# Performance work log

Hardware: AMD Instinct MI355X
Metric: run time of the kernel (lower is better)

Reference implementation:

```python
import jax, jax.numpy as jnp
import numpy as np

HID = 256  # hidden_dim


def setup_inputs() -> dict:
    key = jax.random.key(0)
    ks = jax.random.split(key, 8)
    B, C, H, W = 256, 1, 1024, 64
    D = W  # input_dim
    scale = 0.05
    return {
        "x": jax.random.normal(ks[0], (B, C, H, W), jnp.float32),
        "h0": jax.random.normal(ks[1], (B, HID), jnp.float32),
        "c0": jax.random.normal(ks[2], (B, HID), jnp.float32),
        "Wi": jax.random.normal(ks[3], (4 * HID, D), jnp.float32) * scale,
        "bi": jnp.zeros((4 * HID,), jnp.float32),
        "Wh": jax.random.normal(ks[4], (4 * HID, HID), jnp.float32) * scale,
        "bh": jnp.zeros((4 * HID,), jnp.float32),
        "Wcls": jax.random.normal(ks[5], (10, HID), jnp.float32) * scale,
        "bcls": jnp.zeros((10,), jnp.float32),
    }


def reference(x, h0, c0, Wi, bi, Wh, bh, Wcls, bcls):
    B, C, H, W = x.shape
    S = C * H  # seq_length
    seq = x.reshape(B, S, W)
    # precompute input-to-gate projections for all timesteps: [B,S,4H]
    xg = jnp.einsum("bsd,gd->bsg", seq, Wi) + bi

    def step(carry, xg_t):
        h, c = carry
        g = xg_t + h @ Wh.T + bh  # [B,4H], gate order: f,i,g,o
        f = jax.nn.sigmoid(g[:, 0 * HID:1 * HID])
        i = jax.nn.sigmoid(g[:, 1 * HID:2 * HID])
        gg = jnp.tanh(g[:, 2 * HID:3 * HID])
        o = jax.nn.sigmoid(g[:, 3 * HID:4 * HID])
        c_new = c * f + i * gg
        h_new = jnp.tanh(c_new) * o
        return (h_new, c_new), None

    (h_last, _), _ = jax.lax.scan(step, (h0, c0), jnp.swapaxes(xg, 0, 1))
    # classifier on last hidden state
    return h_last @ Wcls.T + bcls
```

## Files before the change

### kernel.cpp

```cpp
#include <hip/hip_runtime.h>

#define SEQ   1024
#define DIN   64
#define NHID  256
#define NBLK  64
#define NTHR  512

typedef _Float16 f16x8 __attribute__((ext_vector_type(8)));
typedef float    f32x4 __attribute__((ext_vector_type(4)));
typedef unsigned long long u64;

#define MFMA16(a,b,c) __builtin_amdgcn_mfma_f32_16x16x32_f16((a),(b),(c),0,0,0)

__device__ __forceinline__ float sigm(float v){
  return __builtin_amdgcn_rcpf(1.f + __expf(-v));
}
__device__ __forceinline__ float tanh_f(float v){
  return 1.f - 2.f*__builtin_amdgcn_rcpf(__expf(2.f*v)+1.f);
}

__device__ __forceinline__ f16x8 cvt8(f32x4 a, f32x4 b){
  f16x8 r;
  r[0]=(_Float16)a[0]; r[1]=(_Float16)a[1]; r[2]=(_Float16)a[2]; r[3]=(_Float16)a[3];
  r[4]=(_Float16)b[0]; r[5]=(_Float16)b[1]; r[6]=(_Float16)b[2]; r[7]=(_Float16)b[3];
  return r;
}

union U32H2 { unsigned int u; _Float16 h[2]; unsigned short us[2]; };

__global__ void __launch_bounds__(NTHR, 2)
lstm_seq(const float* __restrict__ x, const float* __restrict__ h0,
         const float* __restrict__ c0, const float* __restrict__ Wi,
         const float* __restrict__ bi, const float* __restrict__ Wh,
         const float* __restrict__ bh, const float* __restrict__ Wcls,
         const float* __restrict__ bcls,
         u64* __restrict__ slices, float* __restrict__ out)
{
  __shared__ __align__(16) unsigned int hbuf[2][16*128];

  const int bid = blockIdx.x;
  const int grp = bid & 15;
  const int q   = bid >> 4;
  const int tid = threadIdx.x;
  const int w   = tid >> 6;
  const int l   = tid & 63;
  const int l15 = l & 15;
  const int lhi = l >> 4;

  f16x8 wa[2][8], xa[2][2];
#pragma unroll
  for (int t=0;t<2;t++){
    const int mt  = w*2 + t;
    const int mr  = l15;
    const int jl  = (mt>>1)*8 + ((mr>>2)<<1) + (mt&1);
    const int row = (mr&3)*NHID + q*64 + jl;
#pragma unroll
    for (int kt=0;kt<8;kt++){
      const float* p = Wh + row*NHID + kt*32 + lhi*8;
      wa[t][kt] = cvt8(*(const f32x4*)p, *(const f32x4*)(p+4));
    }
#pragma unroll
    for (int kt=0;kt<2;kt++){
      const float* p = Wi + row*DIN + kt*32 + lhi*8;
      xa[t][kt] = cvt8(*(const f32x4*)p, *(const f32x4*)(p+4));
    }
  }

  f32x4 binit0, binit1; float c[2];
#pragma unroll
  for (int t=0;t<2;t++){
    const int jl = w*8 + lhi*2 + t;
    f32x4 bv;
#pragma unroll
    for (int g=0; g<4; g++)
      bv[g] = bi[g*NHID + q*64 + jl] + bh[g*NHID + q*64 + jl];
    if (t==0) binit0 = bv; else binit1 = bv;
    c[t] = c0[(size_t)(grp*16+l15)*NHID + q*64 + jl];
  }

  for (int i=tid; i<16*128; i+=NTHR){
    const int b = i>>7, cp = i&127;
    U32H2 pk;
    pk.h[0] = (_Float16)h0[(size_t)(grp*16+b)*NHID + cp*2];
    pk.h[1] = (_Float16)h0[(size_t)(grp*16+b)*NHID + cp*2 + 1];
    hbuf[0][i ^ ((b&7)<<2)] = pk.u;
  }
  __syncthreads();

  const float* xrow = x + (size_t)(grp*16 + l15) * (SEQ*DIN);
  f32x4 xp0,xp1,xp2,xp3;
  {
    const float* p = xrow + lhi*8;
    xp0 = *(const f32x4*)p;      xp1 = *(const f32x4*)(p+4);
    xp2 = *(const f32x4*)(p+32); xp3 = *(const f32x4*)(p+36);
  }
  f32x4 acc0, acc1;
  {
    f16x8 xb0 = cvt8(xp0, xp1), xb1 = cvt8(xp2, xp3);
    acc0 = MFMA16(xa[0][0], xb0, binit0);
    acc0 = MFMA16(xa[0][1], xb1, acc0);
    acc1 = MFMA16(xa[1][0], xb0, binit1);
    acc1 = MFMA16(xa[1][1], xb1, acc1);
  }
  {
    const float* p = xrow + DIN + lhi*8;
    xp0 = *(const f32x4*)p;      xp1 = *(const f32x4*)(p+4);
    xp2 = *(const f32x4*)(p+32); xp3 = *(const f32x4*)(p+36);
  }

  for (int s=0; s<SEQ; s++){
    const unsigned int* hr = hbuf[s&1];
    unsigned int*       hw = hbuf[(s+1)&1];

    f16x8 hb[8];
#pragma unroll
    for (int kt=0;kt<8;kt++){
      const int word = (l15*128 + kt*16 + lhi*4) ^ ((l15&7)<<2);
      hb[kt] = *(const f16x8*)(hr + word);
    }
    f32x4 a0 = acc0, a1 = acc1;
    f32x4 b0 = {0.f,0.f,0.f,0.f}, b1 = {0.f,0.f,0.f,0.f};
#pragma unroll
    for (int kt=0;kt<4;kt++){
      a0 = MFMA16(wa[0][kt],   hb[kt],   a0);
      a1 = MFMA16(wa[1][kt],   hb[kt],   a1);
      b0 = MFMA16(wa[0][kt+4], hb[kt+4], b0);
      b1 = MFMA16(wa[1][kt+4], hb[kt+4], b1);
    }
    acc0 = a0 + b0;
    acc1 = a1 + b1;

    U32H2 pk;
    {
      const float f0 = sigm (acc0[0]);
      const float i0 = sigm (acc0[1]);
      const float g0 = tanh_f(acc0[2]);
      const float o0 = sigm (acc0[3]);
      c[0] = c[0]*f0 + i0*g0;
      pk.h[0] = (_Float16)(tanh_f(c[0])*o0);
      const float f1 = sigm (acc1[0]);
      const float i1 = sigm (acc1[1]);
      const float g1 = tanh_f(acc1[2]);
      const float o1 = sigm (acc1[3]);
      c[1] = c[1]*f1 + i1*g1;
      pk.h[1] = (_Float16)(tanh_f(c[1])*o1);
    }
    {
      const u64 word = ((u64)(unsigned)(s+1) << 32) | (u64)pk.u;
      __hip_atomic_store(slices + ((size_t)(s&1)*NBLK + grp*4 + q)*512 + w*64 + l,
                         word, __ATOMIC_RELAXED, __HIP_MEMORY_SCOPE_AGENT);
    }
    {
      const int jp = w*4 + lhi;
      hw[(l15*128 + q*32 + jp) ^ ((l15&7)<<2)] = pk.u;
    }
    {
      f16x8 xb0 = cvt8(xp0, xp1), xb1 = cvt8(xp2, xp3);
      acc0 = MFMA16(xa[0][0], xb0, binit0);
      acc0 = MFMA16(xa[0][1], xb1, acc0);
      acc1 = MFMA16(xa[1][0], xb0, binit1);
      acc1 = MFMA16(xa[1][1], xb1, acc1);
    }
    {
      const int sn = (s < SEQ-2) ? s+2 : SEQ-1;
      const float* p = xrow + sn*DIN + lhi*8;
      xp0 = *(const f32x4*)p;      xp1 = *(const f32x4*)(p+4);
      xp2 = *(const f32x4*)(p+32); xp3 = *(const f32x4*)(p+36);
    }
    const unsigned tag = (unsigned)(s+1);
#pragma unroll
    for (int dq=1; dq<4; dq++){
      const int qq = (q + dq) & 3;
      const u64* sp = slices + ((size_t)(s&1)*NBLK + grp*4 + qq)*512 + w*64 + l;
      u64 v = __hip_atomic_load(sp, __ATOMIC_RELAXED, __HIP_MEMORY_SCOPE_AGENT);
      while ((unsigned)(v >> 32) != tag)
        v = __hip_atomic_load(sp, __ATOMIC_RELAXED, __HIP_MEMORY_SCOPE_AGENT);
      hw[(l15*128 + qq*32 + w*4 + lhi) ^ ((l15&7)<<2)] = (unsigned)v;
    }
    __syncthreads();
  }

  if (q == 0 && tid < 160){
    const int b = tid/10, j = tid - b*10;
    const unsigned int* hf = hbuf[SEQ&1];
    float sum = bcls[j];
    for (int cp=0; cp<128; cp++){
      U32H2 v; v.u = hf[(b*128 + cp) ^ ((b&7)<<2)];
      sum += Wcls[j*NHID + cp*2]     * (float)v.h[0]
           + Wcls[j*NHID + cp*2 + 1] * (float)v.h[1];
    }
    out[(grp*16+b)*10 + j] = sum;
  }
}

extern "C" void kernel_launch(void* const* d_in, const int* in_sizes, int n_in,
                              void* d_out, int out_size, void* d_ws, size_t ws_size,
                              hipStream_t stream){
  const float* x    = (const float*)d_in[0];
  const float* h0   = (const float*)d_in[1];
  const float* c0   = (const float*)d_in[2];
  const float* Wi   = (const float*)d_in[3];
  const float* bi   = (const float*)d_in[4];
  const float* Wh   = (const float*)d_in[5];
  const float* bh   = (const float*)d_in[6];
  const float* Wcls = (const float*)d_in[7];
  const float* bcls = (const float*)d_in[8];

  u64* slices = (u64*)d_ws;

  hipMemsetAsync(slices, 0, 2*NBLK*512*sizeof(u64), stream);
  hipLaunchKernelGGL(lstm_seq, dim3(NBLK), dim3(NTHR), 0, stream,
                     x, h0, c0, Wi, bi, Wh, bh, Wcls, bcls,
                     slices, (float*)d_out);
}
```

Before: 2.138 ms.

## Exchange hidden state through tagged global slices instead of LDS and block barriers

Removes the shared-memory hidden-state buffer and the per-step __syncthreads. Each wave now reads all four quarter-slices of h (its own included) straight from global memory, issuing all 32 loads up front and spinning on the per-word step tags before each MFMA pair. The change is meant to remove the LDS write/read round trip and the block-wide barrier from the serial recurrence critical path. In exchange it adds more global/L2 atomic loads per step and relies on tag polling for correctness; launch bounds also drop to one block per CU.

```diff
diff --git a/kernel.cpp b/kernel.cpp
--- a/kernel.cpp
+++ b/kernel.cpp
@@ -8,9 +8,12 @@
 
 typedef _Float16 f16x8 __attribute__((ext_vector_type(8)));
 typedef float    f32x4 __attribute__((ext_vector_type(4)));
+typedef unsigned int u32x4 __attribute__((ext_vector_type(4)));
 typedef unsigned long long u64;
 
 #define MFMA16(a,b,c) __builtin_amdgcn_mfma_f32_16x16x32_f16((a),(b),(c),0,0,0)
+#define ALOAD(p)   __hip_atomic_load((p), __ATOMIC_RELAXED, __HIP_MEMORY_SCOPE_AGENT)
+#define ASTORE(p,v) __hip_atomic_store((p), (v), __ATOMIC_RELAXED, __HIP_MEMORY_SCOPE_AGENT)
 
 __device__ __forceinline__ float sigm(float v){
   return __builtin_amdgcn_rcpf(1.f + __expf(-v));
@@ -28,7 +31,7 @@
 
 union U32H2 { unsigned int u; _Float16 h[2]; unsigned short us[2]; };
 
-__global__ void __launch_bounds__(NTHR, 2)
+__global__ void __launch_bounds__(NTHR, 1)
 lstm_seq(const float* __restrict__ x, const float* __restrict__ h0,
          const float* __restrict__ c0, const float* __restrict__ Wi,
          const float* __restrict__ bi, const float* __restrict__ Wh,
@@ -36,8 +39,6 @@
          const float* __restrict__ bcls,
          u64* __restrict__ slices, float* __restrict__ out)
 {
-  __shared__ __align__(16) unsigned int hbuf[2][16*128];
-
   const int bid = blockIdx.x;
   const int grp = bid & 15;
   const int q   = bid >> 4;
@@ -78,14 +79,17 @@
     c[t] = c0[(size_t)(grp*16+l15)*NHID + q*64 + jl];
   }
 
-  for (int i=tid; i<16*128; i+=NTHR){
-    const int b = i>>7, cp = i&127;
-    U32H2 pk;
-    pk.h[0] = (_Float16)h0[(size_t)(grp*16+b)*NHID + cp*2];
-    pk.h[1] = (_Float16)h0[(size_t)(grp*16+b)*NHID + cp*2 + 1];
-    hbuf[0][i ^ ((b&7)<<2)] = pk.u;
-  }
-  __syncthreads();
+  u64* gb0 = slices + (size_t)grp*4*512;
+  u64* gb1 = slices + (size_t)NBLK*512 + (size_t)grp*4*512;
+
+  {
+    const int jp = tid >> 4, b = tid & 15;
+    const int col = q*64 + jp*2;
+    U32H2 pk0;
+    pk0.h[0] = (_Float16)h0[(size_t)(grp*16+b)*NHID + col];
+    pk0.h[1] = (_Float16)h0[(size_t)(grp*16+b)*NHID + col+1];
+    ASTORE(gb0 + q*512 + tid, ((u64)1u << 32) | (u64)pk0.u);
+  }
 
   const float* xrow = x + (size_t)(grp*16 + l15) * (SEQ*DIN);
   f32x4 xp0,xp1,xp2,xp3;
@@ -109,51 +113,62 @@
   }
 
   for (int s=0; s<SEQ; s++){
-    const unsigned int* hr = hbuf[s&1];
-    unsigned int*       hw = hbuf[(s+1)&1];
-
-    f16x8 hb[8];
-#pragma unroll
-    for (int kt=0;kt<8;kt++){
-      const int word = (l15*128 + kt*16 + lhi*4) ^ ((l15&7)<<2);
-      hb[kt] = *(const f16x8*)(hr + word);
-    }
+    u64* par = (s&1) ? gb1 : gb0;
+    u64* nxt = (s&1) ? gb0 : gb1;
+    const unsigned tag = (unsigned)(s+1);
+
+    u64 v[4][8];
+#pragma unroll
+    for (int qq=0; qq<4; qq++)
+#pragma unroll
+      for (int h2=0; h2<2; h2++)
+#pragma unroll
+        for (int j=0; j<4; j++)
+          v[qq][h2*4+j] = ALOAD(par + qq*512 + (h2*16 + lhi*4 + j)*16 + l15);
+    __builtin_amdgcn_sched_barrier(0);
+
     f32x4 a0 = acc0, a1 = acc1;
     f32x4 b0 = {0.f,0.f,0.f,0.f}, b1 = {0.f,0.f,0.f,0.f};
 #pragma unroll
-    for (int kt=0;kt<4;kt++){
-      a0 = MFMA16(wa[0][kt],   hb[kt],   a0);
-      a1 = MFMA16(wa[1][kt],   hb[kt],   a1);
-      b0 = MFMA16(wa[0][kt+4], hb[kt+4], b0);
-      b1 = MFMA16(wa[1][kt+4], hb[kt+4], b1);
-    }
-    acc0 = a0 + b0;
-    acc1 = a1 + b1;
+    for (int qq=0; qq<4; qq++){
+      for (;;){
+        bool ok = true;
+#pragma unroll
+        for (int j=0;j<8;j++) ok &= ((unsigned)(v[qq][j] >> 32) == tag);
+        if (ok) break;
+#pragma unroll
+        for (int j=0;j<8;j++)
+          v[qq][j] = ALOAD(par + qq*512 + ((j>>2)*16 + lhi*4 + (j&3))*16 + l15);
+      }
+      u32x4 t0, t1;
+#pragma unroll
+      for (int j=0;j<4;j++){ t0[j] = (unsigned)v[qq][j]; t1[j] = (unsigned)v[qq][4+j]; }
+      const f16x8 f0 = __builtin_bit_cast(f16x8, t0);
+      const f16x8 f1 = __builtin_bit_cast(f16x8, t1);
+      a0 = MFMA16(wa[0][2*qq  ], f0, a0);
+      b0 = MFMA16(wa[0][2*qq+1], f1, b0);
+      a1 = MFMA16(wa[1][2*qq  ], f0, a1);
+      b1 = MFMA16(wa[1][2*qq+1], f1, b1);
+    }
+    const f32x4 g0 = a0 + b0, g1 = a1 + b1;
 
     U32H2 pk;
     {
-      const float f0 = sigm (acc0[0]);
-      const float i0 = sigm (acc0[1]);
-      const float g0 = tanh_f(acc0[2]);
-      const float o0 = sigm (acc0[3]);
-      c[0] = c[0]*f0 + i0*g0;
+      const float f0 = sigm (g0[0]);
+      const float i0 = sigm (g0[1]);
+      const float gg0= tanh_f(g0[2]);
+      const float o0 = sigm (g0[3]);
+      c[0] = c[0]*f0 + i0*gg0;
       pk.h[0] = (_Float16)(tanh_f(c[0])*o0);
-      const float f1 = sigm (acc1[0]);
-      const float i1 = sigm (acc1[1]);
-      const float g1 = tanh_f(acc1[2]);
-      const float o1 = sigm (acc1[3]);
-      c[1] = c[1]*f1 + i1*g1;
+      const float f1 = sigm (g1[0]);
+      const float i1 = sigm (g1[1]);
+      const float gg1= tanh_f(g1[2]);
+      const float o1 = sigm (g1[3]);
+      c[1] = c[1]*f1 + i1*gg1;
       pk.h[1] = (_Float16)(tanh_f(c[1])*o1);
     }
-    {
-      const u64 word = ((u64)(unsigned)(s+1) << 32) | (u64)pk.u;
-      __hip_atomic_store(slices + ((size_t)(s&1)*NBLK + grp*4 + q)*512 + w*64 + l,
-                         word, __ATOMIC_RELAXED, __HIP_MEMORY_SCOPE_AGENT);
-    }
-    {
-      const int jp = w*4 + lhi;
-      hw[(l15*128 + q*32 + jp) ^ ((l15&7)<<2)] = pk.u;
-    }
+    ASTORE(nxt + q*512 + w*64 + l, ((u64)(unsigned)(s+2) << 32) | (u64)pk.u);
+
     {
       f16x8 xb0 = cvt8(xp0, xp1), xb1 = cvt8(xp2, xp3);
       acc0 = MFMA16(xa[0][0], xb0, binit0);
@@ -167,27 +182,19 @@
       xp0 = *(const f32x4*)p;      xp1 = *(const f32x4*)(p+4);
       xp2 = *(const f32x4*)(p+32); xp3 = *(const f32x4*)(p+36);
     }
-    const unsigned tag = (unsigned)(s+1);
-#pragma unroll
-    for (int dq=1; dq<4; dq++){
-      const int qq = (q + dq) & 3;
-      const u64* sp = slices + ((size_t)(s&1)*NBLK + grp*4 + qq)*512 + w*64 + l;
-      u64 v = __hip_atomic_load(sp, __ATOMIC_RELAXED, __HIP_MEMORY_SCOPE_AGENT);
-      while ((unsigned)(v >> 32) != tag)
-        v = __hip_atomic_load(sp, __ATOMIC_RELAXED, __HIP_MEMORY_SCOPE_AGENT);
-      hw[(l15*128 + qq*32 + w*4 + lhi) ^ ((l15&7)<<2)] = (unsigned)v;
-    }
-    __syncthreads();
   }
 
   if (q == 0 && tid < 160){
     const int b = tid/10, j = tid - b*10;
-    const unsigned int* hf = hbuf[SEQ&1];
     float sum = bcls[j];
     for (int cp=0; cp<128; cp++){
-      U32H2 v; v.u = hf[(b*128 + cp) ^ ((b&7)<<2)];
-      sum += Wcls[j*NHID + cp*2]     * (float)v.h[0]
-           + Wcls[j*NHID + cp*2 + 1] * (float)v.h[1];
+      const int qq = cp >> 5, jp = cp & 31;
+      const u64* p = gb0 + qq*512 + jp*16 + b;
+      u64 vv = ALOAD(p);
+      while ((unsigned)(vv >> 32) != (unsigned)(SEQ+1)) vv = ALOAD(p);
+      U32H2 u; u.u = (unsigned)vv;
+      sum += Wcls[j*NHID + cp*2]     * (float)u.h[0]
+           + Wcls[j*NHID + cp*2 + 1] * (float)u.h[1];
     }
     out[(grp*16+b)*10 + j] = sum;
   }
```

Measured after the change: 4.799 ms. +124.5%, slower.

## Split each batch group across two blocks instead of four to cut cross-block exchange

Applied to the files above, without the earlier changes.

Each 16-sample batch group is now split across two workgroups, each owning 128 hidden units, instead of four workgroups owning 64 each. This halves the grid to 32 blocks and doubles per-thread work to four MFMA tiles. Each step now waits on a single partner block rather than three, which shortens the per-step global-memory handshake. Biases move to LDS to ease register pressure, but per-step gate math and MFMA work per thread double, and half as many CUs are used.

```diff
diff --git a/kernel.cpp b/kernel.cpp
--- a/kernel.cpp
+++ b/kernel.cpp
@@ -3,7 +3,7 @@
 #define SEQ   1024
 #define DIN   64
 #define NHID  256
-#define NBLK  64
+#define NBLK  32
 #define NTHR  512
 
 typedef _Float16 f16x8 __attribute__((ext_vector_type(8)));
@@ -11,6 +11,8 @@
 typedef unsigned long long u64;
 
 #define MFMA16(a,b,c) __builtin_amdgcn_mfma_f32_16x16x32_f16((a),(b),(c),0,0,0)
+#define ALOAD(p)    __hip_atomic_load((p), __ATOMIC_RELAXED, __HIP_MEMORY_SCOPE_AGENT)
+#define ASTORE(p,v) __hip_atomic_store((p),(v), __ATOMIC_RELAXED, __HIP_MEMORY_SCOPE_AGENT)
 
 __device__ __forceinline__ float sigm(float v){
   return __builtin_amdgcn_rcpf(1.f + __expf(-v));
@@ -37,23 +39,23 @@
          u64* __restrict__ slices, float* __restrict__ out)
 {
   __shared__ __align__(16) unsigned int hbuf[2][16*128];
+  __shared__ __align__(16) float bini[NTHR*16];
 
   const int bid = blockIdx.x;
   const int grp = bid & 15;
-  const int q   = bid >> 4;
+  const int half= bid >> 4;
   const int tid = threadIdx.x;
   const int w   = tid >> 6;
   const int l   = tid & 63;
   const int l15 = l & 15;
   const int lhi = l >> 4;
 
-  f16x8 wa[2][8], xa[2][2];
-#pragma unroll
-  for (int t=0;t<2;t++){
-    const int mt  = w*2 + t;
-    const int mr  = l15;
-    const int jl  = (mt>>1)*8 + ((mr>>2)<<1) + (mt&1);
-    const int row = (mr&3)*NHID + q*64 + jl;
+  f16x8 wa[4][8], xa[4][2];
+#pragma unroll
+  for (int t=0;t<4;t++){
+    const int mt  = w*4 + t;
+    const int jlA = (mt>>1)*8 + ((l15>>2)<<1) + (mt&1);
+    const int row = (l15&3)*NHID + half*128 + jlA;
 #pragma unroll
     for (int kt=0;kt<8;kt++){
       const float* p = Wh + row*NHID + kt*32 + lhi*8;
@@ -66,16 +68,17 @@
     }
   }
 
-  f32x4 binit0, binit1; float c[2];
-#pragma unroll
-  for (int t=0;t<2;t++){
-    const int jl = w*8 + lhi*2 + t;
+  float c[4];
+#pragma unroll
+  for (int t=0;t<4;t++){
+    const int mt = w*4 + t;
+    const int jl = (mt>>1)*8 + lhi*2 + (mt&1);
+    const int col= half*128 + jl;
     f32x4 bv;
 #pragma unroll
-    for (int g=0; g<4; g++)
-      bv[g] = bi[g*NHID + q*64 + jl] + bh[g*NHID + q*64 + jl];
-    if (t==0) binit0 = bv; else binit1 = bv;
-    c[t] = c0[(size_t)(grp*16+l15)*NHID + q*64 + jl];
+    for (int g=0;g<4;g++) bv[g] = bi[g*NHID + col] + bh[g*NHID + col];
+    *(f32x4*)(bini + tid*16 + t*4) = bv;
+    c[t] = c0[(size_t)(grp*16+l15)*NHID + col];
   }
 
   for (int i=tid; i<16*128; i+=NTHR){
@@ -94,13 +97,14 @@
     xp0 = *(const f32x4*)p;      xp1 = *(const f32x4*)(p+4);
     xp2 = *(const f32x4*)(p+32); xp3 = *(const f32x4*)(p+36);
   }
-  f32x4 acc0, acc1;
+  f32x4 acc[4];
   {
-    f16x8 xb0 = cvt8(xp0, xp1), xb1 = cvt8(xp2, xp3);
-    acc0 = MFMA16(xa[0][0], xb0, binit0);
-    acc0 = MFMA16(xa[0][1], xb1, acc0);
-    acc1 = MFMA16(xa[1][0], xb0, binit1);
-    acc1 = MFMA16(xa[1][1], xb1, acc1);
+    f16x8 xb0 = cvt8(xp0,xp1), xb1 = cvt8(xp2,xp3);
+#pragma unroll
+    for (int t=0;t<4;t++){
+      acc[t] = MFMA16(xa[t][0], xb0, *(const f32x4*)(bini + tid*16 + t*4));
+      acc[t] = MFMA16(xa[t][1], xb1, acc[t]);
+    }
   }
   {
     const float* p = xrow + DIN + lhi*8;
@@ -108,58 +112,55 @@
     xp2 = *(const f32x4*)(p+32); xp3 = *(const f32x4*)(p+36);
   }
 
+  u64* own0 = slices + (size_t)(grp*2 + half)*1024;
+  u64* par0 = slices + (size_t)(grp*2 + (half^1))*1024;
+
   for (int s=0; s<SEQ; s++){
     const unsigned int* hr = hbuf[s&1];
-    unsigned int*       hw = hbuf[(s+1)&1];
-
-    f16x8 hb[8];
+    unsigned int*       hw_= hbuf[(s+1)&1];
+    u64* ownp = own0 + (size_t)(s&1)*NBLK*1024;
+    u64* parp = par0 + (size_t)(s&1)*NBLK*1024;
+    const unsigned tag = (unsigned)(s+1);
+
 #pragma unroll
     for (int kt=0;kt<8;kt++){
       const int word = (l15*128 + kt*16 + lhi*4) ^ ((l15&7)<<2);
-      hb[kt] = *(const f16x8*)(hr + word);
-    }
-    f32x4 a0 = acc0, a1 = acc1;
-    f32x4 b0 = {0.f,0.f,0.f,0.f}, b1 = {0.f,0.f,0.f,0.f};
-#pragma unroll
-    for (int kt=0;kt<4;kt++){
-      a0 = MFMA16(wa[0][kt],   hb[kt],   a0);
-      a1 = MFMA16(wa[1][kt],   hb[kt],   a1);
-      b0 = MFMA16(wa[0][kt+4], hb[kt+4], b0);
-      b1 = MFMA16(wa[1][kt+4], hb[kt+4], b1);
-    }
-    acc0 = a0 + b0;
-    acc1 = a1 + b1;
-
-    U32H2 pk;
-    {
-      const float f0 = sigm (acc0[0]);
-      const float i0 = sigm (acc0[1]);
-      const float g0 = tanh_f(acc0[2]);
-      const float o0 = sigm (acc0[3]);
-      c[0] = c[0]*f0 + i0*g0;
-      pk.h[0] = (_Float16)(tanh_f(c[0])*o0);
-      const float f1 = sigm (acc1[0]);
-      const float i1 = sigm (acc1[1]);
-      const float g1 = tanh_f(acc1[2]);
-      const float o1 = sigm (acc1[3]);
-      c[1] = c[1]*f1 + i1*g1;
-      pk.h[1] = (_Float16)(tanh_f(c[1])*o1);
-    }
-    {
-      const u64 word = ((u64)(unsigned)(s+1) << 32) | (u64)pk.u;
-      __hip_atomic_store(slices + ((size_t)(s&1)*NBLK + grp*4 + q)*512 + w*64 + l,
-                         word, __ATOMIC_RELAXED, __HIP_MEMORY_SCOPE_AGENT);
-    }
-    {
-      const int jp = w*4 + lhi;
-      hw[(l15*128 + q*32 + jp) ^ ((l15&7)<<2)] = pk.u;
-    }
-    {
-      f16x8 xb0 = cvt8(xp0, xp1), xb1 = cvt8(xp2, xp3);
-      acc0 = MFMA16(xa[0][0], xb0, binit0);
-      acc0 = MFMA16(xa[0][1], xb1, acc0);
-      acc1 = MFMA16(xa[1][0], xb0, binit1);
-      acc1 = MFMA16(xa[1][1], xb1, acc1);
+      const f16x8 hb = *(const f16x8*)(hr + word);
+#pragma unroll
+      for (int t=0;t<4;t++) acc[t] = MFMA16(wa[t][kt], hb, acc[t]);
+    }
+
+    U32H2 pk0, pk1;
+    {
+      float hv[4];
+#pragma unroll
+      for (int t=0;t<4;t++){
+        const float f = sigm (acc[t][0]);
+        const float i = sigm (acc[t][1]);
+        const float g = tanh_f(acc[t][2]);
+        const float o = sigm (acc[t][3]);
+        c[t] = c[t]*f + i*g;
+        hv[t] = tanh_f(c[t])*o;
+      }
+      pk0.h[0]=(_Float16)hv[0]; pk0.h[1]=(_Float16)hv[1];
+      pk1.h[0]=(_Float16)hv[2]; pk1.h[1]=(_Float16)hv[3];
+    }
+    ASTORE(ownp + w*128      + l, ((u64)tag<<32) | (u64)pk0.u);
+    ASTORE(ownp + w*128 + 64 + l, ((u64)tag<<32) | (u64)pk1.u);
+    hw_[(l15*128 + half*64 + 8*w   + lhi) ^ ((l15&7)<<2)] = pk0.u;
+    hw_[(l15*128 + half*64 + 8*w+4 + lhi) ^ ((l15&7)<<2)] = pk1.u;
+
+    const u64* pp0 = parp + tid;
+    const u64* pp1 = parp + 512 + tid;
+    u64 v0 = ALOAD(pp0);
+    u64 v1 = ALOAD(pp1);
+    {
+      f16x8 xb0 = cvt8(xp0,xp1), xb1 = cvt8(xp2,xp3);
+#pragma unroll
+      for (int t=0;t<4;t++){
+        acc[t] = MFMA16(xa[t][0], xb0, *(const f32x4*)(bini + tid*16 + t*4));
+        acc[t] = MFMA16(xa[t][1], xb1, acc[t]);
+      }
     }
     {
       const int sn = (s < SEQ-2) ? s+2 : SEQ-1;
@@ -167,20 +168,20 @@
       xp0 = *(const f32x4*)p;      xp1 = *(const f32x4*)(p+4);
       xp2 = *(const f32x4*)(p+32); xp3 = *(const f32x4*)(p+36);
     }
-    const unsigned tag = (unsigned)(s+1);
-#pragma unroll
-    for (int dq=1; dq<4; dq++){
-      const int qq = (q + dq) & 3;
-      const u64* sp = slices + ((size_t)(s&1)*NBLK + grp*4 + qq)*512 + w*64 + l;
-      u64 v = __hip_atomic_load(sp, __ATOMIC_RELAXED, __HIP_MEMORY_SCOPE_AGENT);
-      while ((unsigned)(v >> 32) != tag)
-        v = __hip_atomic_load(sp, __ATOMIC_RELAXED, __HIP_MEMORY_SCOPE_AGENT);
-      hw[(l15*128 + qq*32 + w*4 + lhi) ^ ((l15&7)<<2)] = (unsigned)v;
+    while (((unsigned)(v0>>32) != tag) || ((unsigned)(v1>>32) != tag)){
+      v0 = ALOAD(pp0);
+      v1 = ALOAD(pp1);
+    }
+    {
+      const int ph  = (half^1)*64;
+      const int cpw = tid >> 4;
+      hw_[(l15*128 + ph + cpw)      ^ ((l15&7)<<2)] = (unsigned)v0;
+      hw_[(l15*128 + ph + 32 + cpw) ^ ((l15&7)<<2)] = (unsigned)v1;
     }
     __syncthreads();
   }
 
-  if (q == 0 && tid < 160){
+  if (half == 0 && tid < 160){
     const int b = tid/10, j = tid - b*10;
     const unsigned int* hf = hbuf[SEQ&1];
     float sum = bcls[j];
@@ -208,7 +209,7 @@
 
   u64* slices = (u64*)d_ws;
 
-  hipMemsetAsync(slices, 0, 2*NBLK*512*sizeof(u64), stream);
+  hipMemsetAsync(slices, 0, (size_t)2*NBLK*1024*sizeof(u64), stream);
   hipLaunchKernelGGL(lstm_seq, dim3(NBLK), dim3(NTHR), 0, stream,
                      x, h0, c0, Wi, bi, Wh, bh, Wcls, bcls,
                      slices, (float*)d_out);
```

After: 2.309 ms. +8.0%, slower.
